# Optimization experiments

Measured on AMD Instinct MI355X. Metric: run time of the kernel, lower is better.

## Reference

```python
import jax, jax.numpy as jnp
import numpy as np

K_HEADS, D_HEAD = 8, 8
D = K_HEADS * D_HEAD  # 64


def _fc(x, W, b=None, relu=False):
    # 1x1 Conv2D over (B,T,N,C) == per-position dense
    y = x @ W
    if b is not None:
        y = y + b
    return jax.nn.relu(y) if relu else y


def _split_heads(x):
    # (B,T,N,K*d) -> (K,B,T,N,d); matches torch.cat(torch.split(x, d, -1), 0)
    B, T, N, _ = x.shape
    return x.reshape(B, T, N, K_HEADS, D_HEAD).transpose(3, 0, 1, 2, 4)


def _merge_heads(x):
    # (K,B,T,N,d) -> (B,T,N,K*d); matches torch.cat(torch.split(x, B, 0), -1)
    K, B, T, N, d = x.shape
    return x.transpose(1, 2, 3, 0, 4).reshape(B, T, N, K * d)


def _forward(X, TLE, key_padding_mask, *P):
    (sa_Wq, sa_bq, sa_Wk, sa_bk, sa_Wv, sa_bv, sa_Wo1, sa_bo1, sa_Wo2, sa_bo2,
     ta_Wq, ta_bq, ta_Wk, ta_bk, ta_Wv, ta_bv, ta_Wo1, ta_bo1, ta_Wo2, ta_bo2,
     g_Wxs, g_Wxt, g_bxt, g_Wh1, g_bh1, g_Wh2, g_bh2) = P
    B, T, N, _ = X.shape
    scale = 1.0 / (D_HEAD ** 0.5)
    XE = jnp.concatenate([X, TLE], axis=-1)  # (B,T,N,3D)

    # ---- Spatial attention (over nodes) ----
    q = _split_heads(_fc(XE, sa_Wq, sa_bq, True))
    k = _split_heads(_fc(XE, sa_Wk, sa_bk, True))
    v = _split_heads(_fc(XE, sa_Wv, sa_bv, True))
    s = jnp.einsum('kbtnd,kbtmd->kbtnm', q, k) * scale  # (K,B,T,N,N)
    p = jax.nn.softmax(s, axis=-1)
    HS = _merge_heads(jnp.einsum('kbtnm,kbtmd->kbtnd', p, v))
    HS = _fc(_fc(HS, sa_Wo1, sa_bo1, True), sa_Wo2, sa_bo2)

    # ---- Temporal attention (over time, causal + key padding) ----
    q = _split_heads(_fc(XE, ta_Wq, ta_bq, True))
    k = _split_heads(_fc(XE, ta_Wk, ta_bk, True))
    v = _split_heads(_fc(XE, ta_Wv, ta_bv, True))
    s = jnp.einsum('kbind,kbjnd->kbnij', q, k) * scale  # (K,B,N,T,T)
    causal = jnp.tril(jnp.ones((T, T), dtype=bool))  # (T,T)
    valid_key = jnp.arange(T)[None, :] < key_padding_mask  # (B,T)
    m = causal[None, None, None] & valid_key[None, :, None, None, :]
    s = jnp.where(m, s, -jnp.inf)
    p = jax.nn.softmax(s, axis=-1)
    HT = _merge_heads(jnp.einsum('kbnij,kbjnd->kbind', p, v))
    HT = _fc(_fc(HT, ta_Wo1, ta_bo1, True), ta_Wo2, ta_bo2)

    # ---- Gated fusion + residual ----
    z = jax.nn.sigmoid(HS @ g_Wxs + HT @ g_Wxt + g_bxt)
    H = z * HS + (1.0 - z) * HT
    H = _fc(_fc(H, g_Wh1, g_bh1, True), g_Wh2, g_bh2)
    return X + H


_PARAM_SHAPES = []
for _pre in ('sa', 'ta'):
    _PARAM_SHAPES += [(_pre + '_Wq', (3 * D, D)), (_pre + '_bq', (D,)),
                      (_pre + '_Wk', (3 * D, D)), (_pre + '_bk', (D,)),
                      (_pre + '_Wv', (3 * D, D)), (_pre + '_bv', (D,)),
                      (_pre + '_Wo1', (D, D)), (_pre + '_bo1', (D,)),
                      (_pre + '_Wo2', (D, D)), (_pre + '_bo2', (D,))]
_PARAM_SHAPES += [('g_Wxs', (D, D)), ('g_Wxt', (D, D)), ('g_bxt', (D,)),
                  ('g_Wh1', (D, D)), ('g_bh1', (D,)),
                  ('g_Wh2', (D, D)), ('g_bh2', (D,))]


def setup_inputs() -> dict:
    key = jax.random.key(0)
    ks = jax.random.split(key, 3 + len(_PARAM_SHAPES))
    B, T, N = 16, 24, 128
    inp = {
        'X': jax.random.normal(ks[0], (B, T, N, D), dtype=jnp.float32),
        'TLE': jax.random.normal(ks[1], (B, T, N, 2 * D), dtype=jnp.float32),
        'key_padding_mask': jax.random.randint(ks[2], (B, 1), 1, T + 1),
    }
    for i, (nm, shp) in enumerate(_PARAM_SHAPES):
        inp[nm] = jax.random.normal(ks[3 + i], shp, dtype=jnp.float32) * 0.05
    return inp


def reference(X, TLE, key_padding_mask,
              sa_Wq, sa_bq, sa_Wk, sa_bk, sa_Wv, sa_bv, sa_Wo1, sa_bo1, sa_Wo2, sa_bo2,
              ta_Wq, ta_bq, ta_Wk, ta_bk, ta_Wv, ta_bv, ta_Wo1, ta_bo1, ta_Wo2, ta_bo2,
              g_Wxs, g_Wxt, g_bxt, g_Wh1, g_bh1, g_Wh2, g_bh2):
    return _forward(X, TLE, key_padding_mask,
                    sa_Wq, sa_bq, sa_Wk, sa_bk, sa_Wv, sa_bv, sa_Wo1, sa_bo1, sa_Wo2, sa_bo2,
                    ta_Wq, ta_bq, ta_Wk, ta_bk, ta_Wv, ta_bv, ta_Wo1, ta_bo1, ta_Wo2, ta_bo2,
                    g_Wxs, g_Wxt, g_bxt, g_Wh1, g_bh1, g_Wh2, g_bh2)
```

## Files before the change

kernel.cpp:

```cpp
#include <hip/hip_runtime.h>
#include <math.h>

#define BB 16
#define TT 24
#define NN 128
#define DD 64
#define PTOT (BB * TT * NN)
#define P64  (PTOT * 64)

typedef __attribute__((ext_vector_type(8))) short bf16x8;
typedef __attribute__((ext_vector_type(4))) float f32x4;
typedef __attribute__((ext_vector_type(16))) float f32x16;

__device__ __forceinline__ unsigned short f2bf(float f) {
    unsigned u = __builtin_bit_cast(unsigned, f);
    u = (u + 0x7fffu + ((u >> 16) & 1u)) >> 16;
    return (unsigned short)u;
}
__device__ __forceinline__ void unpack8(uint4 u, float* f) {
    f[0] = __builtin_bit_cast(float, u.x << 16);
    f[1] = __builtin_bit_cast(float, u.x & 0xFFFF0000u);
    f[2] = __builtin_bit_cast(float, u.y << 16);
    f[3] = __builtin_bit_cast(float, u.y & 0xFFFF0000u);
    f[4] = __builtin_bit_cast(float, u.z << 16);
    f[5] = __builtin_bit_cast(float, u.z & 0xFFFF0000u);
    f[6] = __builtin_bit_cast(float, u.w << 16);
    f[7] = __builtin_bit_cast(float, u.w & 0xFFFF0000u);
}
__device__ __forceinline__ uint4 pack8(const float* f) {
    uint4 o;
    o.x = (unsigned)f2bf(f[0]) | ((unsigned)f2bf(f[1]) << 16);
    o.y = (unsigned)f2bf(f[2]) | ((unsigned)f2bf(f[3]) << 16);
    o.z = (unsigned)f2bf(f[4]) | ((unsigned)f2bf(f[5]) << 16);
    o.w = (unsigned)f2bf(f[6]) | ((unsigned)f2bf(f[7]) << 16);
    return o;
}
__device__ __forceinline__ float fast_exp2(float x) {
#if __has_builtin(__builtin_amdgcn_exp2f)
    return __builtin_amdgcn_exp2f(x);
#else
    return exp2f(x);
#endif
}
__device__ __forceinline__ unsigned cvt_pk_bf16(float a, float b) {
    unsigned r;
    asm("v_cvt_pk_bf16_f32 %0, %1, %2" : "=v"(r) : "v"(a), "v"(b));
    return r;
}
__device__ __forceinline__ f32x16 zero16() {
    f32x16 z;
    #pragma unroll
    for (int i = 0; i < 16; ++i) z[i] = 0.f;
    return z;
}

__global__ __launch_bounds__(256) void wprep_all(
    const float* __restrict__ W0, const float* __restrict__ W1,
    const float* __restrict__ W2, const float* __restrict__ W3,
    const float* __restrict__ W4, const float* __restrict__ W5,
    const float* __restrict__ E0, const float* __restrict__ E1,
    const float* __restrict__ E2, const float* __restrict__ E3,
    const float* __restrict__ E4, const float* __restrict__ E5,
    const float* __restrict__ E6, const float* __restrict__ E7,
    unsigned short* __restrict__ Wt, unsigned short* __restrict__ Wt8)
{
    const int bid = blockIdx.x;
    if (bid < 288) {
        const float* Ws[6] = {W0, W1, W2, W3, W4, W5};
        const int e = bid * 256 + threadIdx.x;
        const int j = e / 12288;
        const int r = e % 12288;
        const int k = r / 64;
        const int n = r % 64;
        Wt[j * 12288 + n * 192 + k] = f2bf(Ws[j][k * 64 + n]);
    } else {
        const float* Es[8] = {E0, E1, E2, E3, E4, E5, E6, E7};
        const int e = (bid - 288) * 256 + threadIdx.x;
        const int mat = e >> 12;
        const int r = e & 4095;
        const int k = r >> 6;
        const int n = r & 63;
        Wt8[mat * 4096 + n * 64 + k] = f2bf(Es[mat][k * 64 + n]);
    }
}

__global__ __launch_bounds__(256, 2) void fused_sattn(
    const float* __restrict__ X, const float* __restrict__ TLE,
    const unsigned short* __restrict__ Wt,
    const float* __restrict__ b0, const float* __restrict__ b1,
    const float* __restrict__ b2, const float* __restrict__ b3,
    const float* __restrict__ b4, const float* __restrict__ b5,
    unsigned short* __restrict__ qt, unsigned short* __restrict__ kt,
    unsigned short* __restrict__ vt,
    unsigned short* __restrict__ HS)
{
    __shared__ __align__(16) unsigned short xe[2][16][200];
    __shared__ __align__(16) unsigned short qq[128 * 64];
    __shared__ __align__(16) unsigned short kk[128 * 64];
    __shared__ __align__(16) unsigned short vv[128 * 64];
    const int tid = threadIdx.x;
    const long p0 = (long)blockIdx.x * 128;
    const int w = tid >> 6, l = tid & 63, quad = l >> 4, l16 = l & 15;

    auto stage = [&](int mt, int buf) {
        #pragma unroll
        for (int i = 0; i < 3; ++i) {
            const int idx4 = tid + i * 256;
            const int m  = idx4 / 48;
            const int kq = idx4 % 48;
            const int k  = kq * 4;
            const long p = p0 + mt * 16 + m;
            float4 v;
            if (k < 64) v = *reinterpret_cast<const float4*>(X + p * 64 + k);
            else        v = *reinterpret_cast<const float4*>(TLE + p * 128 + (k - 64));
            ushort4 pk;
            pk.x = f2bf(v.x); pk.y = f2bf(v.y); pk.z = f2bf(v.z); pk.w = f2bf(v.w);
            *reinterpret_cast<ushort4*>(&xe[buf][m][k]) = pk;
        }
    };

    bf16x8 wf[6][6];
    #pragma unroll
    for (int mat = 0; mat < 6; ++mat)
        #pragma unroll
        for (int kc = 0; kc < 6; ++kc)
            wf[mat][kc] = *reinterpret_cast<const bf16x8*>(
                &Wt[mat * 12288 + (w * 16 + l16) * 192 + kc * 32 + quad * 8]);

    const float* bias_p[6] = {b0, b1, b2, b3, b4, b5};
    float4 bias[6];
    #pragma unroll
    for (int mat = 0; mat < 6; ++mat)
        bias[mat] = *reinterpret_cast<const float4*>(&bias_p[mat][w * 16 + quad * 4]);

    stage(0, 0);
    __syncthreads();

    const int chunkW = ((w * 2 + (quad >> 1)));
    const int chSub  = (quad & 1) * 4;
    const int chBase = w * 16 + quad * 4;
    const float cs = 0.35355339059327373f * 1.4426950408889634f;

    for (int mt = 0; mt < 8; ++mt) {
        if (mt < 7) stage(mt + 1, (mt + 1) & 1);

        bf16x8 A[6];
        #pragma unroll
        for (int kc = 0; kc < 6; ++kc)
            A[kc] = *reinterpret_cast<const bf16x8*>(
                &xe[mt & 1][l16][kc * 32 + quad * 8]);

        f32x4 acc[6];
        #pragma unroll
        for (int mat = 0; mat < 6; ++mat) acc[mat] = (f32x4){0.f, 0.f, 0.f, 0.f};
        #pragma unroll
        for (int kc = 0; kc < 6; ++kc)
            #pragma unroll
            for (int mat = 0; mat < 6; ++mat)
                acc[mat] = __builtin_amdgcn_mfma_f32_16x16x32_bf16(
                    wf[mat][kc], A[kc], acc[mat], 0, 0, 0);

        const int pos = mt * 16 + l16;
        const int sw  = pos * 64 + ((chunkW ^ (pos & 7)) << 3) + chSub;
        unsigned short* dstS[3] = {qq, kk, vv};
        #pragma unroll
        for (int mat = 0; mat < 3; ++mat) {
            const float sc = (mat == 0) ? cs : 1.0f;
            ushort4 pk;
            pk.x = f2bf(fmaxf(acc[mat][0] + bias[mat].x, 0.f) * sc);
            pk.y = f2bf(fmaxf(acc[mat][1] + bias[mat].y, 0.f) * sc);
            pk.z = f2bf(fmaxf(acc[mat][2] + bias[mat].z, 0.f) * sc);
            pk.w = f2bf(fmaxf(acc[mat][3] + bias[mat].w, 0.f) * sc);
            *reinterpret_cast<ushort4*>(&dstS[mat][sw]) = pk;
        }
        unsigned short* dstT[3] = {qt, kt, vt};
        const long gp = (p0 + pos) * 64 + chBase;
        #pragma unroll
        for (int m3 = 3; m3 < 6; ++m3) {
            ushort4 pk;
            pk.x = f2bf(fmaxf(acc[m3][0] + bias[m3].x, 0.f));
            pk.y = f2bf(fmaxf(acc[m3][1] + bias[m3].y, 0.f));
            pk.z = f2bf(fmaxf(acc[m3][2] + bias[m3].z, 0.f));
            pk.w = f2bf(fmaxf(acc[m3][3] + bias[m3].w, 0.f));
            *reinterpret_cast<ushort4*>(&dstT[m3 - 3][gp]) = pk;
        }
        __syncthreads();
    }

    const int hi = l >> 5;
    const int ln = l & 31;
    bf16x8 zf = {};

    auto pvstep = [&](f32x16& st, const bf16x8& va0, const bf16x8& va1,
                      f32x16& oacc) {
        const unsigned P0 = cvt_pk_bf16(st[0],  st[1]);
        const unsigned P1 = cvt_pk_bf16(st[2],  st[3]);
        const unsigned P2 = cvt_pk_bf16(st[4],  st[5]);
        const unsigned P3 = cvt_pk_bf16(st[6],  st[7]);
        const unsigned P4 = cvt_pk_bf16(st[8],  st[9]);
        const unsigned P5 = cvt_pk_bf16(st[10], st[11]);
        const unsigned P6 = cvt_pk_bf16(st[12], st[13]);
        const unsigned P7 = cvt_pk_bf16(st[14], st[15]);
        const unsigned V0 = __shfl_xor(hi ? P0 : P2, 32);
        const unsigned V1 = __shfl_xor(hi ? P1 : P3, 32);
        const unsigned V2 = __shfl_xor(hi ? P4 : P6, 32);
        const unsigned V3 = __shfl_xor(hi ? P5 : P7, 32);
        uint4 fe, fo;
        fe.x = hi ? V0 : P0; fe.y = hi ? V1 : P1;
        fe.z = hi ? P2 : V0; fe.w = hi ? P3 : V1;
        fo.x = hi ? V2 : P4; fo.y = hi ? V3 : P5;
        fo.z = hi ? P6 : V2; fo.w = hi ? P7 : V3;
        oacc = __builtin_amdgcn_mfma_f32_32x32x16_bf16(
            va0, __builtin_bit_cast(bf16x8, fe), oacc, 0, 0, 0);
        oacc = __builtin_amdgcn_mfma_f32_32x32x16_bf16(
            va1, __builtin_bit_cast(bf16x8, fo), oacc, 0, 0, 0);
    };

    #pragma unroll
    for (int hh2 = 0; hh2 < 2; ++hh2) {
        const int h = w * 2 + hh2;
        const int swz = (h ^ (ln & 7)) << 3;

        bf16x8 kf0 = hi ? zf : *reinterpret_cast<const bf16x8*>(&kk[(0 * 32 + ln) * 64 + swz]);
        bf16x8 kf1 = hi ? zf : *reinterpret_cast<const bf16x8*>(&kk[(1 * 32 + ln) * 64 + swz]);
        bf16x8 kf2 = hi ? zf : *reinterpret_cast<const bf16x8*>(&kk[(2 * 32 + ln) * 64 + swz]);
        bf16x8 kf3 = hi ? zf : *reinterpret_cast<const bf16x8*>(&kk[(3 * 32 + ln) * 64 + swz]);

        bf16x8 vf[8];
        #pragma unroll
        for (int c = 0; c < 8; ++c) {
            bf16x8 f = zf;
            if (ln < 8) {
                #pragma unroll
                for (int j = 0; j < 8; ++j) {
                    const int m = c * 16 + hi * 8 + j;
                    f[j] = (short)vv[m * 64 + ((h ^ (m & 7)) << 3) + ln];
                }
            }
            vf[c] = f;
        }

        #pragma unroll
        for (int nt = 0; nt < 4; ++nt) {
            const int qrow = nt * 32 + ln;
            bf16x8 qf = hi ? zf : *reinterpret_cast<const bf16x8*>(&qq[qrow * 64 + swz]);

            f32x16 st0 = zero16(), st1 = zero16(), st2 = zero16(), st3 = zero16();
            st0 = __builtin_amdgcn_mfma_f32_32x32x16_bf16(kf0, qf, st0, 0, 0, 0);
            st1 = __builtin_amdgcn_mfma_f32_32x32x16_bf16(kf1, qf, st1, 0, 0, 0);
            st2 = __builtin_amdgcn_mfma_f32_32x32x16_bf16(kf2, qf, st2, 0, 0, 0);
            st3 = __builtin_amdgcn_mfma_f32_32x32x16_bf16(kf3, qf, st3, 0, 0, 0);

            float sum = 0.f;
            #pragma unroll
            for (int r = 0; r < 16; ++r) { st0[r] = fast_exp2(st0[r]); sum += st0[r]; }
            #pragma unroll
            for (int r = 0; r < 16; ++r) { st1[r] = fast_exp2(st1[r]); sum += st1[r]; }
            #pragma unroll
            for (int r = 0; r < 16; ++r) { st2[r] = fast_exp2(st2[r]); sum += st2[r]; }
            #pragma unroll
            for (int r = 0; r < 16; ++r) { st3[r] = fast_exp2(st3[r]); sum += st3[r]; }
            sum += __shfl_xor(sum, 32);

            f32x16 oacc = zero16();
            pvstep(st0, vf[0], vf[1], oacc);
            pvstep(st1, vf[2], vf[3], oacc);
            pvstep(st2, vf[4], vf[5], oacc);
            pvstep(st3, vf[6], vf[7], oacc);

            const float inv = 1.0f / sum;
            ushort4 pk;
            pk.x = f2bf(oacc[0] * inv);
            pk.y = f2bf(oacc[1] * inv);
            pk.z = f2bf(oacc[2] * inv);
            pk.w = f2bf(oacc[3] * inv);
            *reinterpret_cast<ushort4*>(&HS[(p0 + qrow) * 64 + h * 8 + hi * 4]) = pk;
        }
    }
}

__global__ __launch_bounds__(192) void tattn_kernel(
    const unsigned short* __restrict__ Q, const unsigned short* __restrict__ Kb,
    const unsigned short* __restrict__ V, const int* __restrict__ kpm,
    unsigned short* __restrict__ O)
{
    __shared__ float kk[8][TT][8];
    __shared__ float vv[8][TT][8];
    const int tid = threadIdx.x;
    const int n = blockIdx.x & (NN - 1);
    const int b = blockIdx.x >> 7;

    {
        const int hs = tid / TT;
        const int j  = tid % TT;
        const long g = (((long)(b * TT + j)) * NN + n) * 64 + hs * 8;
        uint4 ku = *reinterpret_cast<const uint4*>(&Kb[g]);
        uint4 vu = *reinterpret_cast<const uint4*>(&V[g]);
        float kf[8], vf[8];
        unpack8(ku, kf); unpack8(vu, vf);
        #pragma unroll
        for (int d = 0; d < 8; ++d) { kk[hs][j][d] = kf[d]; vv[hs][j][d] = vf[d]; }
    }

    const int h = tid / TT;
    const int i = tid % TT;
    const long qb = (((long)(b * TT + i)) * NN + n) * 64 + h * 8;
    float q[8];
    {
        uint4 qu = *reinterpret_cast<const uint4*>(&Q[qb]);
        unpack8(qu, q);
    }
    __syncthreads();

    const int kp = kpm[b];
    const float scale = 0.35355339059327373f;

    float s[TT];
    #pragma unroll
    for (int j = 0; j < TT; ++j) {
        float t = 0.0f;
        #pragma unroll
        for (int d = 0; d < 8; ++d) t = fmaf(q[d], kk[h][j][d], t);
        s[j] = (j <= i && j < kp) ? t * scale : -INFINITY;
    }
    float mx = -INFINITY;
    #pragma unroll
    for (int j = 0; j < TT; ++j) mx = fmaxf(mx, s[j]);

    float sum = 0.0f;
    float acc[8];
    #pragma unroll
    for (int d = 0; d < 8; ++d) acc[d] = 0.0f;
    #pragma unroll
    for (int j = 0; j < TT; ++j) {
        const float e = __expf(s[j] - mx);
        sum += e;
        #pragma unroll
        for (int d = 0; d < 8; ++d) acc[d] = fmaf(e, vv[h][j][d], acc[d]);
    }
    const float inv = 1.0f / sum;
    float o[8];
    #pragma unroll
    for (int d = 0; d < 8; ++d) o[d] = acc[d] * inv;
    *reinterpret_cast<uint4*>(&O[qb]) = pack8(o);
}

__global__ __launch_bounds__(256) void epi_kernel(
    const float* __restrict__ X,
    const unsigned short* __restrict__ HSb, const unsigned short* __restrict__ HTb,
    const unsigned short* __restrict__ Wt8,
    const float* __restrict__ sbo1, const float* __restrict__ sbo2,
    const float* __restrict__ tbo1, const float* __restrict__ tbo2,
    const float* __restrict__ bxt,
    const float* __restrict__ bh1, const float* __restrict__ bh2,
    float* __restrict__ out)
{
    constexpr int RS = 72;
    __shared__ __align__(16) unsigned short bufA[64][RS], bufB[64][RS], bufC[64][RS];
    const int tid = threadIdx.x;
    const long p0 = (long)blockIdx.x * 64;
    const int w = tid >> 6, l = tid & 63, quad = l >> 4, l16 = l & 15;
    const int chBase = w * 16 + quad * 4;

    #pragma unroll
    for (int i = 0; i < 4; ++i) {
        const int idx = tid + i * 256;
        const int m = idx >> 4;
        const int c = (idx & 15) * 4;
        *reinterpret_cast<ushort4*>(&bufA[m][c]) =
            *reinterpret_cast<const ushort4*>(&HSb[(p0 + m) * 64 + c]);
        *reinterpret_cast<ushort4*>(&bufC[m][c]) =
            *reinterpret_cast<const ushort4*>(&HTb[(p0 + m) * 64 + c]);
    }
    __syncthreads();

    auto gemm = [&](const unsigned short (*in)[RS], int mat,
                    const float* __restrict__ bias, f32x4* accO) {
        bf16x8 af[2];
        #pragma unroll
        for (int kc = 0; kc < 2; ++kc)
            af[kc] = *reinterpret_cast<const bf16x8*>(
                &Wt8[mat * 4096 + (w * 16 + l16) * 64 + kc * 32 + quad * 8]);
        const float4 b4 = *reinterpret_cast<const float4*>(&bias[chBase]);
        #pragma unroll
        for (int pt = 0; pt < 4; ++pt) {
            f32x4 acc = (f32x4){0.f, 0.f, 0.f, 0.f};
            #pragma unroll
            for (int kc = 0; kc < 2; ++kc) {
                bf16x8 bf = *reinterpret_cast<const bf16x8*>(
                    &in[pt * 16 + l16][kc * 32 + quad * 8]);
                acc = __builtin_amdgcn_mfma_f32_16x16x32_bf16(af[kc], bf, acc, 0, 0, 0);
            }
            acc[0] += b4.x; acc[1] += b4.y; acc[2] += b4.z; acc[3] += b4.w;
            accO[pt] = acc;
        }
    };

    auto writeBuf = [&](unsigned short (*dst)[RS], const f32x4* v, bool relu) {
        #pragma unroll
        for (int pt = 0; pt < 4; ++pt) {
            float a0 = v[pt][0], a1 = v[pt][1], a2 = v[pt][2], a3 = v[pt][3];
            if (relu) { a0 = fmaxf(a0, 0.f); a1 = fmaxf(a1, 0.f);
                        a2 = fmaxf(a2, 0.f); a3 = fmaxf(a3, 0.f); }
            ushort4 pk; pk.x = f2bf(a0); pk.y = f2bf(a1); pk.z = f2bf(a2); pk.w = f2bf(a3);
            *reinterpret_cast<ushort4*>(&dst[pt * 16 + l16][chBase]) = pk;
        }
    };

    f32x4 t[4], HSr[4], HTr[4];

    gemm(bufA, 0, sbo1, t);
    __syncthreads();
    writeBuf(bufB, t, true);
    __syncthreads();

    gemm(bufB, 1, sbo2, HSr);
    __syncthreads();
    writeBuf(bufA, HSr, false);
    __syncthreads();

    gemm(bufC, 2, tbo1, t);
    __syncthreads();
    writeBuf(bufB, t, true);
    __syncthreads();

    gemm(bufB, 3, tbo2, HTr);
    __syncthreads();
    writeBuf(bufC, HTr, false);
    __syncthreads();

    {
        bf16x8 afS[2], afT[2];
        #pragma unroll
        for (int kc = 0; kc < 2; ++kc) {
            afS[kc] = *reinterpret_cast<const bf16x8*>(
                &Wt8[4 * 4096 + (w * 16 + l16) * 64 + kc * 32 + quad * 8]);
            afT[kc] = *reinterpret_cast<const bf16x8*>(
                &Wt8[5 * 4096 + (w * 16 + l16) * 64 + kc * 32 + quad * 8]);
        }
        const float4 b4 = *reinterpret_cast<const float4*>(&bxt[chBase]);
        #pragma unroll
        for (int pt = 0; pt < 4; ++pt) {
            f32x4 acc = (f32x4){0.f, 0.f, 0.f, 0.f};
            #pragma unroll
            for (int kc = 0; kc < 2; ++kc) {
                bf16x8 hsf = *reinterpret_cast<const bf16x8*>(
                    &bufA[pt * 16 + l16][kc * 32 + quad * 8]);
                acc = __builtin_amdgcn_mfma_f32_16x16x32_bf16(afS[kc], hsf, acc, 0, 0, 0);
            }
            #pragma unroll
            for (int kc = 0; kc < 2; ++kc) {
                bf16x8 htf = *reinterpret_cast<const bf16x8*>(
                    &bufC[pt * 16 + l16][kc * 32 + quad * 8]);
                acc = __builtin_amdgcn_mfma_f32_16x16x32_bf16(afT[kc], htf, acc, 0, 0, 0);
            }
            const float zb[4] = {acc[0] + b4.x, acc[1] + b4.y, acc[2] + b4.z, acc[3] + b4.w};
            f32x4 h;
            #pragma unroll
            for (int r = 0; r < 4; ++r) {
                const float z = 1.0f / (1.0f + __expf(-zb[r]));
                h[r] = z * HSr[pt][r] + (1.0f - z) * HTr[pt][r];
            }
            t[pt] = h;
        }
    }
    __syncthreads();
    writeBuf(bufB, t, false);
    __syncthreads();

    gemm(bufB, 6, bh1, t);
    __syncthreads();
    writeBuf(bufA, t, true);
    __syncthreads();

    gemm(bufA, 7, bh2, t);
    #pragma unroll
    for (int pt = 0; pt < 4; ++pt) {
        const long pos = p0 + pt * 16 + l16;
        const float4 xv = *reinterpret_cast<const float4*>(&X[pos * 64 + chBase]);
        float4 o;
        o.x = t[pt][0] + xv.x; o.y = t[pt][1] + xv.y;
        o.z = t[pt][2] + xv.z; o.w = t[pt][3] + xv.w;
        *reinterpret_cast<float4*>(&out[pos * 64 + chBase]) = o;
    }
}

extern "C" void kernel_launch(void* const* d_in, const int* in_sizes, int n_in,
                              void* d_out, int out_size, void* d_ws, size_t ws_size,
                              hipStream_t stream) {
    const float* X   = (const float*)d_in[0];
    const float* TLE = (const float*)d_in[1];
    const int* kpm   = (const int*)d_in[2];

    const float* sa_Wq = (const float*)d_in[3];  const float* sa_bq = (const float*)d_in[4];
    const float* sa_Wk = (const float*)d_in[5];  const float* sa_bk = (const float*)d_in[6];
    const float* sa_Wv = (const float*)d_in[7];  const float* sa_bv = (const float*)d_in[8];
    const float* sa_Wo1 = (const float*)d_in[9];  const float* sa_bo1 = (const float*)d_in[10];
    const float* sa_Wo2 = (const float*)d_in[11]; const float* sa_bo2 = (const float*)d_in[12];
    const float* ta_Wq = (const float*)d_in[13]; const float* ta_bq = (const float*)d_in[14];
    const float* ta_Wk = (const float*)d_in[15]; const float* ta_bk = (const float*)d_in[16];
    const float* ta_Wv = (const float*)d_in[17]; const float* ta_bv = (const float*)d_in[18];
    const float* ta_Wo1 = (const float*)d_in[19]; const float* ta_bo1 = (const float*)d_in[20];
    const float* ta_Wo2 = (const float*)d_in[21]; const float* ta_bo2 = (const float*)d_in[22];
    const float* g_Wxs = (const float*)d_in[23];
    const float* g_Wxt = (const float*)d_in[24]; const float* g_bxt = (const float*)d_in[25];
    const float* g_Wh1 = (const float*)d_in[26]; const float* g_bh1 = (const float*)d_in[27];
    const float* g_Wh2 = (const float*)d_in[28]; const float* g_bh2 = (const float*)d_in[29];

    unsigned short* wsp = (unsigned short*)d_ws;
    unsigned short* qt  = wsp + 0L * P64;
    unsigned short* kt  = wsp + 1L * P64;
    unsigned short* vt  = wsp + 2L * P64;
    unsigned short* HSb = wsp + 3L * P64;
    unsigned short* HTb = wsp + 4L * P64;
    unsigned short* Wt  = wsp + 5L * P64;
    unsigned short* Wt8 = Wt + 6 * 12288;

    float* out = (float*)d_out;

    hipLaunchKernelGGL(wprep_all, dim3(416), dim3(256), 0, stream,
                       sa_Wq, sa_Wk, sa_Wv, ta_Wq, ta_Wk, ta_Wv,
                       sa_Wo1, sa_Wo2, ta_Wo1, ta_Wo2, g_Wxs, g_Wxt, g_Wh1, g_Wh2,
                       Wt, Wt8);

    hipLaunchKernelGGL(fused_sattn, dim3(BB * TT), dim3(256), 0, stream,
                       X, TLE, Wt,
                       sa_bq, sa_bk, sa_bv, ta_bq, ta_bk, ta_bv,
                       qt, kt, vt, HSb);

    hipLaunchKernelGGL(tattn_kernel, dim3(BB * NN), dim3(192), 0, stream,
                       qt, kt, vt, kpm, HTb);

    hipLaunchKernelGGL(epi_kernel, dim3(PTOT / 64), dim3(256), 0, stream,
                       X, HSb, HTb, Wt8,
                       sa_bo1, sa_bo2, ta_bo1, ta_bo2, g_bxt, g_bh1, g_bh2,
                       out);
}
```

Measured before the change: 82.42 us.

## Keep Q in registers via cross-lane shuffles to raise spatial-attention occupancy

Removes the shared-memory Q buffer in the fused spatial attention kernel. Each lane instead packs its scaled Q projections into registers and rebuilds the MFMA Q fragments with wave shuffles. The smaller LDS footprint allows launch bounds of three blocks per CU. The barrier per tile becomes a raw s_barrier with an lgkmcnt wait and is skipped on the last tile, and the tile loop is fully unrolled. In exchange it adds many shuffles and a tighter register budget, which may cause spills.

```diff
diff --git a/kernel.cpp b/kernel.cpp
--- a/kernel.cpp
+++ b/kernel.cpp
@@ -84,7 +84,7 @@
     }
 }
 
-__global__ __launch_bounds__(256, 2) void fused_sattn(
+__global__ __launch_bounds__(256, 3) void fused_sattn(
     const float* __restrict__ X, const float* __restrict__ TLE,
     const unsigned short* __restrict__ Wt,
     const float* __restrict__ b0, const float* __restrict__ b1,
@@ -95,7 +95,6 @@
     unsigned short* __restrict__ HS)
 {
     __shared__ __align__(16) unsigned short xe[2][16][200];
-    __shared__ __align__(16) unsigned short qq[128 * 64];
     __shared__ __align__(16) unsigned short kk[128 * 64];
     __shared__ __align__(16) unsigned short vv[128 * 64];
     const int tid = threadIdx.x;
@@ -141,6 +140,9 @@
     const int chBase = w * 16 + quad * 4;
     const float cs = 0.35355339059327373f * 1.4426950408889634f;
 
+    unsigned qpk[16];
+
+    #pragma unroll
     for (int mt = 0; mt < 8; ++mt) {
         if (mt < 7) stage(mt + 1, (mt + 1) & 1);
 
@@ -161,17 +163,23 @@
                     wf[mat][kc], A[kc], acc[mat], 0, 0, 0);
 
         const int pos = mt * 16 + l16;
+        qpk[2 * mt + 0] =
+            (unsigned)f2bf(fmaxf(acc[0][0] + bias[0].x, 0.f) * cs) |
+            ((unsigned)f2bf(fmaxf(acc[0][1] + bias[0].y, 0.f) * cs) << 16);
+        qpk[2 * mt + 1] =
+            (unsigned)f2bf(fmaxf(acc[0][2] + bias[0].z, 0.f) * cs) |
+            ((unsigned)f2bf(fmaxf(acc[0][3] + bias[0].w, 0.f) * cs) << 16);
+
         const int sw  = pos * 64 + ((chunkW ^ (pos & 7)) << 3) + chSub;
-        unsigned short* dstS[3] = {qq, kk, vv};
-        #pragma unroll
-        for (int mat = 0; mat < 3; ++mat) {
-            const float sc = (mat == 0) ? cs : 1.0f;
+        unsigned short* dstS[2] = {kk, vv};
+        #pragma unroll
+        for (int mat = 1; mat <= 2; ++mat) {
             ushort4 pk;
-            pk.x = f2bf(fmaxf(acc[mat][0] + bias[mat].x, 0.f) * sc);
-            pk.y = f2bf(fmaxf(acc[mat][1] + bias[mat].y, 0.f) * sc);
-            pk.z = f2bf(fmaxf(acc[mat][2] + bias[mat].z, 0.f) * sc);
-            pk.w = f2bf(fmaxf(acc[mat][3] + bias[mat].w, 0.f) * sc);
-            *reinterpret_cast<ushort4*>(&dstS[mat][sw]) = pk;
+            pk.x = f2bf(fmaxf(acc[mat][0] + bias[mat].x, 0.f));
+            pk.y = f2bf(fmaxf(acc[mat][1] + bias[mat].y, 0.f));
+            pk.z = f2bf(fmaxf(acc[mat][2] + bias[mat].z, 0.f));
+            pk.w = f2bf(fmaxf(acc[mat][3] + bias[mat].w, 0.f));
+            *reinterpret_cast<ushort4*>(&dstS[mat - 1][sw]) = pk;
         }
         unsigned short* dstT[3] = {qt, kt, vt};
         const long gp = (p0 + pos) * 64 + chBase;
@@ -184,12 +192,37 @@
             pk.w = f2bf(fmaxf(acc[m3][3] + bias[m3].w, 0.f));
             *reinterpret_cast<ushort4*>(&dstT[m3 - 3][gp]) = pk;
         }
-        __syncthreads();
+        if (mt < 7) {
+            __builtin_amdgcn_sched_barrier(0);
+            asm volatile("s_waitcnt lgkmcnt(0)" ::: "memory");
+            __builtin_amdgcn_s_barrier();
+            __builtin_amdgcn_sched_barrier(0);
+        }
     }
 
     const int hi = l >> 5;
     const int ln = l & 31;
     bf16x8 zf = {};
+
+    auto qfrag = [&](int hh2, int nt) -> bf16x8 {
+        const int s0 = hh2 * 32 + (ln & 15);
+        const int s1 = s0 + 16;
+        const bool odd = (ln >> 4) & 1;
+        const unsigned a0 = __shfl(qpk[4 * nt + 0], s0, 64);
+        const unsigned a1 = __shfl(qpk[4 * nt + 2], s0, 64);
+        const unsigned b0 = __shfl(qpk[4 * nt + 1], s0, 64);
+        const unsigned b1 = __shfl(qpk[4 * nt + 3], s0, 64);
+        const unsigned c0 = __shfl(qpk[4 * nt + 0], s1, 64);
+        const unsigned c1 = __shfl(qpk[4 * nt + 2], s1, 64);
+        const unsigned e0 = __shfl(qpk[4 * nt + 1], s1, 64);
+        const unsigned e1 = __shfl(qpk[4 * nt + 3], s1, 64);
+        uint4 u;
+        u.x = odd ? a1 : a0;
+        u.y = odd ? b1 : b0;
+        u.z = odd ? c1 : c0;
+        u.w = odd ? e1 : e0;
+        return hi ? zf : __builtin_bit_cast(bf16x8, u);
+    };
 
     auto pvstep = [&](f32x16& st, const bf16x8& va0, const bf16x8& va1,
                       f32x16& oacc) {
@@ -243,7 +276,7 @@
         #pragma unroll
         for (int nt = 0; nt < 4; ++nt) {
             const int qrow = nt * 32 + ln;
-            bf16x8 qf = hi ? zf : *reinterpret_cast<const bf16x8*>(&qq[qrow * 64 + swz]);
+            bf16x8 qf = qfrag(hh2, nt);
 
             f32x16 st0 = zero16(), st1 = zero16(), st2 = zero16(), st3 = zero16();
             st0 = __builtin_amdgcn_mfma_f32_32x32x16_bf16(kf0, qf, st0, 0, 0, 0);
```

New measurement: 129.7 us. 57.4% more time.
